# Optimization experiments

Hardware: AMD Instinct MI355X
Metric: run time of the kernel (lower is better)

Reference implementation:

```python
import jax, jax.numpy as jnp
import numpy as np


def setup_inputs() -> dict:
    key = jax.random.key(0)
    B, S, H, O, L, NH = 16, 1024, 1024, 256, 4, 8
    ks = jax.random.split(key, 10)
    s = 0.02
    return {
        "x": jax.random.normal(ks[0], (B, S, H), dtype=jnp.float32),
        "Wf": jax.random.normal(ks[1], (L, H, H), dtype=jnp.float32) * s,
        "bf": jnp.zeros((L, H), dtype=jnp.float32),
        "Wi": jax.random.normal(ks[2], (L, H, H), dtype=jnp.float32) * s,
        "bi": jnp.zeros((L, H), dtype=jnp.float32),
        "Wh": jax.random.normal(ks[3], (L, H, H), dtype=jnp.float32) * s,
        "bh": jnp.zeros((L, H), dtype=jnp.float32),
        "in_proj_w": jax.random.normal(ks[4], (3 * H, H), dtype=jnp.float32) * s,
        "in_proj_b": jnp.zeros((3 * H,), dtype=jnp.float32),
        "out_w": jax.random.normal(ks[5], (H, H), dtype=jnp.float32) * s,
        "out_b": jnp.zeros((H,), dtype=jnp.float32),
        "fc_w": jax.random.normal(ks[6], (O, H), dtype=jnp.float32) * s,
        "fc_b": jnp.zeros((O,), dtype=jnp.float32),
    }


def _min_lstm_layer(x, Wf, bf, Wi, bi, Wh, bh):
    # x: [B, S, D] -> [B, S, H]. minLSTM: h_t = f'_t * h_{t-1} + i'_t * h~_t
    f = jax.nn.sigmoid(jnp.einsum("bsd,hd->bsh", x, Wf) + bf)
    i = jax.nn.sigmoid(jnp.einsum("bsd,hd->bsh", x, Wi) + bi)
    h_tilde = jnp.einsum("bsd,hd->bsh", x, Wh) + bh
    denom = f + i
    fp = f / denom                      # decay coefficient per step
    add = (i / denom) * h_tilde         # input contribution per step
    # sequential scan over time (linear gated recurrence)
    def step(h, inp):
        fp_t, add_t = inp               # each [B, H]
        h = fp_t * h + add_t
        return h, h
    B, S, H = fp.shape
    h0 = jnp.zeros((B, H), dtype=x.dtype)
    _, hs = jax.lax.scan(step, h0, (fp.transpose(1, 0, 2), add.transpose(1, 0, 2)))
    return hs.transpose(1, 0, 2)        # [B, S, H]


def _mhsa(x, in_proj_w, in_proj_b, out_w, out_b, num_heads=8):
    B, S, H = x.shape
    dh = H // num_heads
    qkv = jnp.einsum("bsh,oh->bso", x, in_proj_w) + in_proj_b  # [B,S,3H]
    q, k, v = jnp.split(qkv, 3, axis=-1)
    def heads(t):
        return t.reshape(B, S, num_heads, dh).transpose(0, 2, 1, 3)  # [B,nh,S,dh]
    q, k, v = heads(q), heads(k), heads(v)
    scores = jnp.einsum("bnqd,bnkd->bnqk", q, k) / jnp.sqrt(jnp.float32(dh)).astype(x.dtype)
    attn = jax.nn.softmax(scores, axis=-1)
    o = jnp.einsum("bnqk,bnkd->bnqd", attn, v)
    o = o.transpose(0, 2, 1, 3).reshape(B, S, H)
    return jnp.einsum("bsh,oh->bso", o, out_w) + out_b


def reference(x, Wf, bf, Wi, bi, Wh, bh, in_proj_w, in_proj_b, out_w, out_b, fc_w, fc_b):
    out = x
    L = Wf.shape[0]
    for l in range(L):
        out = _min_lstm_layer(out, Wf[l], bf[l], Wi[l], bi[l], Wh[l], bh[l])
    attn_out = _mhsa(out, in_proj_w, in_proj_b, out_w, out_b, num_heads=8)
    out = attn_out + out                 # dropout is identity at eval
    last = out[:, -1, :]                 # [B, H]
    return jnp.einsum("bh,oh->bo", last, fc_w) + fc_b
```

## Files before the change

### kernel.cpp

```cpp
#include <hip/hip_runtime.h>
#include <hip/hip_bf16.h>
#include <math.h>

#define Bq   16
#define Sq   1024
#define Hq   1024
#define Oq   256
#define Lq   4
#define NHq  8
#define DHq  128
#define Mq   (Bq*Sq)
#define HHq  (Hq*Hq)
#define NCc  32
#define CTc  32

typedef __bf16 bf16x8 __attribute__((ext_vector_type(8)));
typedef float  f32x4  __attribute__((ext_vector_type(4)));

__device__ __forceinline__ float bf2f(unsigned int u) {
    union { unsigned int i; float f; } x; x.i = u << 16; return x.f;
}
__device__ __forceinline__ unsigned short f2bf(float f) {
    union { float f; unsigned int i; } x; x.f = f;
    unsigned int r = x.i + 0x7fffu + ((x.i >> 16) & 1u);
    return (unsigned short)(r >> 16);
}
__device__ __forceinline__ float sigm(float x) { return 1.f / (1.f + __expf(-x)); }

__device__ __forceinline__ void gl2lds16(const unsigned short* g, unsigned short* l) {
    __builtin_amdgcn_global_load_lds((const __attribute__((address_space(1))) void*)g,
                                     (__attribute__((address_space(3))) void*)l, 16, 0, 0);
}

__global__ void cvt_kernel(const float* __restrict__ src, unsigned short* __restrict__ dst, int n) {
    int i = blockIdx.x * 256 + threadIdx.x;
    if (i < n) dst[i] = f2bf(src[i]);
}

__global__ void cvtW_kernel(const float* __restrict__ Wf, const float* __restrict__ Wi,
                            const float* __restrict__ Wh, unsigned short* __restrict__ Wcat) {
    int i = blockIdx.x * 256 + threadIdx.x;
    int l = (i >> 20) / 3;
    int r = i - l * 3 * HHq;
    int g = r >> 20; int j = r & (HHq - 1);
    const float* s = (g == 0) ? Wf : (g == 1) ? Wi : Wh;
    Wcat[i] = f2bf(s[(size_t)l * HHq + j]);
}

__global__ void bias3_kernel(const float* __restrict__ bf_, const float* __restrict__ bi_,
                             const float* __restrict__ bh_, float* __restrict__ out) {
    int i = blockIdx.x * 256 + threadIdx.x;
    int l = i / (3*Hq); int r = i % (3*Hq); int g = r >> 10; int j = r & (Hq-1);
    const float* s = (g == 0) ? bf_ : (g == 1) ? bi_ : bh_;
    out[i] = s[l*Hq + j];
}

__global__ __launch_bounds__(256, 3)
void gemm_gate_kernel(const unsigned short* __restrict__ A, const unsigned short* __restrict__ Wl,
                      const float* __restrict__ bias3, unsigned short* __restrict__ FPo,
                      unsigned short* __restrict__ ADDo)
{
    const int K = Hq;
    __shared__ unsigned short As[2*4096];
    __shared__ unsigned short Ws[2*6144];
    const int tid  = threadIdx.x;

    const int lid = blockIdx.x;
    const int xcd = lid & 7;
    const int s   = lid >> 3;
    const int bm  = xcd * 16 + (s >> 4);
    const int cb  = s & 15;

    const int wid  = tid >> 6, lane = tid & 63;
    const int wm   = (wid >> 1) * 64;
    const int wn   = (wid & 1) * 32;
    const int l15  = lane & 15, quad = lane >> 4;

    const unsigned short* Ag = A + (size_t)(bm*128) * K;

    const int lr   = lane >> 2;
    const int gc   = (lane & 3) ^ ((lane >> 3) & 3);
    size_t offA[2]; int ldsA[2];
    #pragma unroll
    for (int q = 0; q < 2; ++q) {
        int ra = wid*32 + q*16 + lr;
        offA[q] = (size_t)ra * K + gc*8;
        ldsA[q] = (wid*32 + q*16) * 32;
    }
    size_t offW[3]; int ldsW[3];
    #pragma unroll
    for (int q = 0; q < 3; ++q) {
        int rw = wid*48 + q*16 + lr;
        int g  = rw >> 6;
        int nr = rw & 63;
        offW[q] = (size_t)g * HHq + (size_t)(cb*64 + nr) * K + gc*8;
        ldsW[q] = (wid*48 + q*16) * 32;
    }

    const int crd = quad ^ ((l15 >> 1) & 3);

    f32x4 acc[3][4][2] = {};

    const int niter = K >> 5;

    #pragma unroll
    for (int q = 0; q < 2; ++q) gl2lds16(Ag + offA[q], &As[ldsA[q]]);
    #pragma unroll
    for (int q = 0; q < 3; ++q) gl2lds16(Wl + offW[q], &Ws[ldsW[q]]);
    __syncthreads();

    for (int it = 0; it < niter; ++it) {
        const int cur = it & 1;
        if (it + 1 < niter) {
            const int nxt = (it + 1) & 1;
            const size_t k1 = (size_t)(it + 1) << 5;
            #pragma unroll
            for (int q = 0; q < 2; ++q) gl2lds16(Ag + offA[q] + k1, &As[nxt*4096 + ldsA[q]]);
            #pragma unroll
            for (int q = 0; q < 3; ++q) gl2lds16(Wl + offW[q] + k1, &Ws[nxt*6144 + ldsW[q]]);
        }
        bf16x8 af[4];
        #pragma unroll
        for (int t = 0; t < 4; ++t)
            af[t] = *(const bf16x8*)&As[cur*4096 + (wm + t*16 + l15)*32 + crd*8];
        #pragma unroll
        for (int g = 0; g < 3; ++g) {
            bf16x8 wf[2];
            #pragma unroll
            for (int t = 0; t < 2; ++t)
                wf[t] = *(const bf16x8*)&Ws[cur*6144 + (g*64 + wn + t*16 + l15)*32 + crd*8];
            #pragma unroll
            for (int tm = 0; tm < 4; ++tm)
                #pragma unroll
                for (int tn = 0; tn < 2; ++tn)
                    acc[g][tm][tn] = __builtin_amdgcn_mfma_f32_16x16x32_bf16(af[tm], wf[tn], acc[g][tm][tn], 0, 0, 0);
        }
        __syncthreads();
    }

    #pragma unroll
    for (int tm = 0; tm < 4; ++tm) {
        int row0 = bm*128 + wm + tm*16 + quad*4;
        #pragma unroll
        for (int tn = 0; tn < 2; ++tn) {
            int col = cb*64 + wn + tn*16 + l15;
            float bf_ = bias3[col], bi_ = bias3[Hq + col], bh_ = bias3[2*Hq + col];
            #pragma unroll
            for (int r = 0; r < 4; ++r) {
                float f  = sigm(acc[0][tm][tn][r] + bf_);
                float i  = sigm(acc[1][tm][tn][r] + bi_);
                float ht = acc[2][tm][tn][r] + bh_;
                float rd = 1.f / (f + i);
                size_t off = (size_t)(row0 + r) * Hq + col;
                FPo[off]  = f2bf(f * rd);
                ADDo[off] = f2bf(i * rd * ht);
            }
        }
    }
}

__global__ __launch_bounds__(256)
void gemm_bt_kernel(const unsigned short* __restrict__ A, const unsigned short* __restrict__ W,
                    const float* __restrict__ bias, unsigned short* __restrict__ C,
                    int N, int K, int nbn)
{
    __shared__ unsigned short As[2*4096];
    __shared__ unsigned short Ws[2*4096];
    const int tid  = threadIdx.x;

    const int lid = blockIdx.x;
    const int xcd = lid & 7;
    const int s   = lid >> 3;
    const int bm  = xcd * 16 + s / nbn;
    const int bn  = s % nbn;

    const int wid  = tid >> 6, lane = tid & 63;
    const int wm   = (wid >> 1) * 64, wn = (wid & 1) * 64;
    const int l15  = lane & 15, quad = lane >> 4;

    const unsigned short* Ag = A + (size_t)(bm*128) * K;
    const unsigned short* Wg = W + (size_t)(bn*128) * K;

    const int r0   = wid*32 + (lane >> 2);
    const int cst  = (lane & 3) ^ ((r0 >> 1) & 3);
    const size_t g0 = (size_t)r0 * K + cst*8;
    const size_t g1 = (size_t)(r0 + 16) * K + cst*8;
    const int lofs0 = wid*1024;
    const int lofs1 = wid*1024 + 512;

    const int crd = quad ^ ((l15 >> 1) & 3);

    f32x4 acc[4][4] = {};

    const int niter = K >> 5;

    gl2lds16(Ag + g0, &As[lofs0]);
    gl2lds16(Ag + g1, &As[lofs1]);
    gl2lds16(Wg + g0, &Ws[lofs0]);
    gl2lds16(Wg + g1, &Ws[lofs1]);
    __syncthreads();

    for (int it = 0; it < niter; ++it) {
        const int cur = it & 1;
        if (it + 1 < niter) {
            const int nxt = (it + 1) & 1;
            const size_t k1 = (size_t)(it + 1) << 5;
            gl2lds16(Ag + g0 + k1, &As[nxt*4096 + lofs0]);
            gl2lds16(Ag + g1 + k1, &As[nxt*4096 + lofs1]);
            gl2lds16(Wg + g0 + k1, &Ws[nxt*4096 + lofs0]);
            gl2lds16(Wg + g1 + k1, &Ws[nxt*4096 + lofs1]);
        }
        bf16x8 af[4], wf[4];
        #pragma unroll
        for (int t = 0; t < 4; ++t) {
            af[t] = *(const bf16x8*)&As[cur*4096 + (wm + t*16 + l15)*32 + crd*8];
            wf[t] = *(const bf16x8*)&Ws[cur*4096 + (wn + t*16 + l15)*32 + crd*8];
        }
        #pragma unroll
        for (int tm = 0; tm < 4; ++tm)
            #pragma unroll
            for (int tn = 0; tn < 4; ++tn)
                acc[tm][tn] = __builtin_amdgcn_mfma_f32_16x16x32_bf16(af[tm], wf[tn], acc[tm][tn], 0, 0, 0);
        __syncthreads();
    }

    #pragma unroll
    for (int tm = 0; tm < 4; ++tm) {
        int row0 = bm*128 + wm + tm*16 + quad*4;
        #pragma unroll
        for (int tn = 0; tn < 4; ++tn) {
            int col = bn*128 + wn + tn*16 + l15;
            float bv = bias[col];
            #pragma unroll
            for (int r = 0; r < 4; ++r)
                C[(size_t)(row0 + r) * N + col] = f2bf(acc[tm][tn][r] + bv);
        }
    }
}

__global__ __launch_bounds__(256)
void scan_sum_kernel(const unsigned short* __restrict__ FP, const unsigned short* __restrict__ AD,
                     float* __restrict__ Ps, float* __restrict__ Asum) {
    int bid = blockIdx.x;
    int tid = threadIdx.x;
    int b = bid >> 6; int r = bid & 63; int chunk = r >> 1; int jb = r & 1;
    int j = jb*512 + tid*2;
    size_t base = ((size_t)(b*Sq + chunk*CTc)) * Hq + j;
    float P0 = 1.f, P1 = 1.f, A0 = 0.f, A1 = 0.f;
    for (int s = 0; s < CTc; ++s) {
        size_t ro = base + (size_t)s * Hq;
        unsigned int uf = *(const unsigned int*)(FP + ro);
        unsigned int ua = *(const unsigned int*)(AD + ro);
        float fp0 = bf2f(uf & 0xffffu), fp1 = bf2f(uf >> 16);
        float ad0 = bf2f(ua & 0xffffu), ad1 = bf2f(ua >> 16);
        P0 *= fp0; A0 = fp0 * A0 + ad0;
        P1 *= fp1; A1 = fp1 * A1 + ad1;
    }
    int oi = (b*NCc + chunk)*Hq + j;
    Ps[oi] = P0; Ps[oi+1] = P1;
    Asum[oi] = A0; Asum[oi+1] = A1;
}

__global__ void scan_base_kernel(const float* __restrict__ Ps, const float* __restrict__ Asum,
                                 float* __restrict__ Hb) {
    int t = blockIdx.x * 256 + threadIdx.x;
    int b = t >> 10, j = t & 1023;
    float h = 0.f;
    for (int c = 0; c < NCc; ++c) {
        int idx = (b*NCc + c)*Hq + j;
        Hb[idx] = h;
        h = Ps[idx] * h + Asum[idx];
    }
}

__global__ __launch_bounds__(256)
void scan_out_kernel(const unsigned short* __restrict__ FP, const unsigned short* __restrict__ AD,
                     const float* __restrict__ Hb, unsigned short* __restrict__ Ho) {
    int bid = blockIdx.x;
    int tid = threadIdx.x;
    int b = bid >> 6; int r = bid & 63; int chunk = r >> 1; int jb = r & 1;
    int j = jb*512 + tid*2;
    size_t base = ((size_t)(b*Sq + chunk*CTc)) * Hq + j;
    int oi = (b*NCc + chunk)*Hq + j;
    float h0 = Hb[oi], h1 = Hb[oi+1];
    for (int s = 0; s < CTc; ++s) {
        size_t ro = base + (size_t)s * Hq;
        unsigned int uf = *(const unsigned int*)(FP + ro);
        unsigned int ua = *(const unsigned int*)(AD + ro);
        h0 = bf2f(uf & 0xffffu) * h0 + bf2f(ua & 0xffffu);
        h1 = bf2f(uf >> 16)     * h1 + bf2f(ua >> 16);
        unsigned int packed = (unsigned int)f2bf(h0) | ((unsigned int)f2bf(h1) << 16);
        *(unsigned int*)(Ho + ro) = packed;
    }
}

__global__ void xlast_kernel(const unsigned short* __restrict__ act, float* __restrict__ xl) {
    int i = blockIdx.x * 256 + threadIdx.x;
    int b = i >> 10, j = i & 1023;
    xl[i] = bf2f((unsigned int)act[((size_t)(b*Sq + Sq-1)) * Hq + j]);
}

__global__ __launch_bounds__(256)
void gemv_kernel(const float* __restrict__ W, const float* __restrict__ xv,
                 const float* __restrict__ bias, const float* __restrict__ resid,
                 float* __restrict__ out, int N) {
    int b = blockIdx.x;
    int w = threadIdx.x >> 6, lane = threadIdx.x & 63;
    int n = blockIdx.y*4 + w;
    __shared__ float xs[Hq];
    *(float4*)&xs[threadIdx.x*4] = *(const float4*)&xv[(size_t)b*Hq + threadIdx.x*4];
    __syncthreads();
    const float4* wr = (const float4*)(W + (size_t)n * Hq);
    float a = 0.f;
    #pragma unroll
    for (int c = 0; c < 4; ++c) {
        float4 wv = wr[c*64 + lane];
        float4 x4 = *(const float4*)&xs[c*256 + lane*4];
        a += wv.x*x4.x + wv.y*x4.y + wv.z*x4.z + wv.w*x4.w;
    }
    #pragma unroll
    for (int st = 32; st > 0; st >>= 1) a += __shfl_xor(a, st, 64);
    if (lane == 0) out[(size_t)b*N + n] = a + bias[n] + (resid ? resid[(size_t)b*Hq + n] : 0.f);
}

__global__ __launch_bounds__(1024)
void attn_kernel(const unsigned short* __restrict__ KV,
                 const float* __restrict__ q, float* __restrict__ o) {
    int b = blockIdx.x >> 3, nh = blockIdx.x & 7;
    int tid = threadIdx.x;
    __shared__ float qs[DHq];
    __shared__ float p[Sq];
    __shared__ float redw[16];
    __shared__ float red2[16*DHq];
    if (tid < DHq) qs[tid] = q[b*Hq + nh*DHq + tid] * 0.08838834764831845f;
    __syncthreads();

    const int g = tid >> 4, l = tid & 15;
    const unsigned short* Kb = KV + (size_t)b*Sq*2048 + nh*DHq;
    float lmax = -1e30f;
    #pragma unroll 4
    for (int it = 0; it < 16; ++it) {
        int s = it*64 + g;
        union { uint4 v; unsigned short u[8]; } kk;
        kk.v = *(const uint4*)(Kb + (size_t)s*2048 + l*8);
        float a = 0.f;
        #pragma unroll
        for (int j = 0; j < 8; ++j) a += bf2f((unsigned int)kk.u[j]) * qs[l*8 + j];
        a += __shfl_xor(a, 1, 16);
        a += __shfl_xor(a, 2, 16);
        a += __shfl_xor(a, 4, 16);
        a += __shfl_xor(a, 8, 16);
        if (l == 0) p[s] = a;
        lmax = fmaxf(lmax, a);
    }
    #pragma unroll
    for (int st = 32; st > 0; st >>= 1) lmax = fmaxf(lmax, __shfl_xor(lmax, st, 64));
    if ((tid & 63) == 0) redw[tid >> 6] = lmax;
    __syncthreads();
    float mx = redw[0];
    #pragma unroll
    for (int i = 1; i < 16; ++i) mx = fmaxf(mx, redw[i]);

    float e = __expf(p[tid] - mx);
    float ls = e;
    #pragma unroll
    for (int st = 32; st > 0; st >>= 1) ls += __shfl_xor(ls, st, 64);
    __syncthreads();
    p[tid] = e;
    if ((tid & 63) == 0) redw[tid >> 6] = ls;
    __syncthreads();
    float ssum = 0.f;
    #pragma unroll
    for (int i = 0; i < 16; ++i) ssum += redw[i];
    float inv = 1.f / ssum;

    int d2 = (tid & 63) * 2, sb = tid >> 6;
    const unsigned short* Vb = KV + (size_t)b*Sq*2048 + 1024 + nh*DHq + d2;
    float a0 = 0.f, a1 = 0.f;
    for (int s = sb*64; s < sb*64 + 64; ++s) {
        unsigned int vv = *(const unsigned int*)(Vb + (size_t)s*2048);
        float pw = p[s];
        a0 += pw * bf2f(vv & 0xffffu);
        a1 += pw * bf2f(vv >> 16);
    }
    red2[sb*DHq + d2] = a0;
    red2[sb*DHq + d2 + 1] = a1;
    __syncthreads();
    if (tid < DHq) {
        float a = 0.f;
        #pragma unroll
        for (int i = 0; i < 16; ++i) a += red2[i*DHq + tid];
        o[b*Hq + nh*DHq + tid] = a * inv;
    }
}

extern "C" void kernel_launch(void* const* d_in, const int* in_sizes, int n_in,
                              void* d_out, int out_size, void* d_ws, size_t ws_size,
                              hipStream_t stream) {
    const float* x        = (const float*)d_in[0];
    const float* Wf       = (const float*)d_in[1];
    const float* bfv      = (const float*)d_in[2];
    const float* Wi       = (const float*)d_in[3];
    const float* biv      = (const float*)d_in[4];
    const float* Wh       = (const float*)d_in[5];
    const float* bhv      = (const float*)d_in[6];
    const float* in_proj_w= (const float*)d_in[7];
    const float* in_proj_b= (const float*)d_in[8];
    const float* out_w    = (const float*)d_in[9];
    const float* out_b    = (const float*)d_in[10];
    const float* fc_w     = (const float*)d_in[11];
    const float* fc_b     = (const float*)d_in[12];
    float* outp = (float*)d_out;

    char* p = (char*)d_ws;
    auto alloc = [&](size_t bytes) -> void* {
        void* r = (void*)p; p += (bytes + 255) & ~(size_t)255; return r;
    };
    unsigned short* Wcat = (unsigned short*)alloc((size_t)Lq*3*HHq*2);
    unsigned short* Wkv  = (unsigned short*)alloc((size_t)2048*Hq*2);
    float*          Bias3= (float*)alloc((size_t)Lq*3*Hq*4);
    unsigned short* actA = (unsigned short*)alloc((size_t)Mq*Hq*2);
    unsigned short* actB = (unsigned short*)alloc((size_t)Mq*Hq*2);
    unsigned short* FPg  = (unsigned short*)alloc((size_t)Mq*Hq*2);
    unsigned short* ADDg = (unsigned short*)alloc((size_t)Mq*Hq*2);
    float* Ps   = (float*)alloc((size_t)Bq*NCc*Hq*4);
    float* Asum = (float*)alloc((size_t)Bq*NCc*Hq*4);
    float* Hb   = (float*)alloc((size_t)Bq*NCc*Hq*4);
    unsigned short* KV = FPg;
    float* xl   = (float*)alloc((size_t)Bq*Hq*4);
    float* qbuf = (float*)alloc((size_t)Bq*Hq*4);
    float* obuf = (float*)alloc((size_t)Bq*Hq*4);
    float* rbuf = (float*)alloc((size_t)Bq*Hq*4);

    cvt_kernel<<<Mq*Hq/256, 256, 0, stream>>>(x, actA, Mq*Hq);
    cvtW_kernel<<<Lq*3*HHq/256, 256, 0, stream>>>(Wf, Wi, Wh, Wcat);
    cvt_kernel<<<2048*Hq/256, 256, 0, stream>>>(in_proj_w + (size_t)Hq*Hq, Wkv, 2048*Hq);
    bias3_kernel<<<(Lq*3*Hq)/256, 256, 0, stream>>>(bfv, biv, bhv, Bias3);

    unsigned short* cur = actA;
    unsigned short* nxt = actB;
    for (int l = 0; l < Lq; ++l) {
        gemm_gate_kernel<<<(Mq/128)*16, 256, 0, stream>>>(
            cur, Wcat + (size_t)l*3*HHq, Bias3 + l*3*Hq, FPg, ADDg);
        scan_sum_kernel<<<Bq*NCc*2, 256, 0, stream>>>(FPg, ADDg, Ps, Asum);
        scan_base_kernel<<<Bq*Hq/256, 256, 0, stream>>>(Ps, Asum, Hb);
        scan_out_kernel<<<Bq*NCc*2, 256, 0, stream>>>(FPg, ADDg, Hb, nxt);
        unsigned short* t = cur; cur = nxt; nxt = t;
    }

    gemm_bt_kernel<<<(Mq/128)*(2048/128), 256, 0, stream>>>(
        cur, Wkv, in_proj_b + Hq, KV, 2048, Hq, 2048/128);
    xlast_kernel<<<Bq*Hq/256, 256, 0, stream>>>(cur, xl);
    gemv_kernel<<<dim3(Bq, Hq/4), 256, 0, stream>>>(in_proj_w, xl, in_proj_b, nullptr, qbuf, Hq);
    attn_kernel<<<Bq*NHq, 1024, 0, stream>>>(KV, qbuf, obuf);
    gemv_kernel<<<dim3(Bq, Hq/4), 256, 0, stream>>>(out_w, obuf, out_b, xl, rbuf, Hq);
    gemv_kernel<<<dim3(Bq, Oq/4), 256, 0, stream>>>(fc_w, rbuf, fc_b, nullptr, outp, Oq);
}
```

Measured before the change: 917.9 us.

## Enlarge gate GEMM tile to 128x384 with 512 threads and 4-stage LDS pipeline

The fused gate GEMM now uses 512-thread blocks covering 128 hidden columns per gate instead of 64, which halves the grid and increases reuse of A tiles. The double-buffered loop is replaced by a 4-slot LDS ring with two stages prefetched ahead, explicit vmcnt waits and raw barriers, and s_setprio raised around the MFMA block. This aims to hide global-load latency and cut per-tile overhead, at the cost of 128KB of LDS per block and lower occupancy.

```diff
diff --git a/kernel.cpp b/kernel.cpp
--- a/kernel.cpp
+++ b/kernel.cpp
@@ -55,95 +55,107 @@
     out[i] = s[l*Hq + j];
 }
 
-__global__ __launch_bounds__(256, 3)
+__global__ __launch_bounds__(512, 2)
 void gemm_gate_kernel(const unsigned short* __restrict__ A, const unsigned short* __restrict__ Wl,
                       const float* __restrict__ bias3, unsigned short* __restrict__ FPo,
                       unsigned short* __restrict__ ADDo)
 {
     const int K = Hq;
-    __shared__ unsigned short As[2*4096];
-    __shared__ unsigned short Ws[2*6144];
+    __shared__ unsigned short lds[4 * 16384];
     const int tid  = threadIdx.x;
 
     const int lid = blockIdx.x;
     const int xcd = lid & 7;
     const int s   = lid >> 3;
-    const int bm  = xcd * 16 + (s >> 4);
-    const int cb  = s & 15;
+    const int bm  = xcd * 16 + (s >> 3);
+    const int cb  = s & 7;
 
     const int wid  = tid >> 6, lane = tid & 63;
-    const int wm   = (wid >> 1) * 64;
-    const int wn   = (wid & 1) * 32;
+    const int wm   = (wid >> 2) * 64;
+    const int wn   = (wid & 3) * 32;
     const int l15  = lane & 15, quad = lane >> 4;
 
     const unsigned short* Ag = A + (size_t)(bm*128) * K;
 
-    const int lr   = lane >> 2;
-    const int gc   = (lane & 3) ^ ((lane >> 3) & 3);
-    size_t offA[2]; int ldsA[2];
-    #pragma unroll
-    for (int q = 0; q < 2; ++q) {
-        int ra = wid*32 + q*16 + lr;
-        offA[q] = (size_t)ra * K + gc*8;
-        ldsA[q] = (wid*32 + q*16) * 32;
-    }
-    size_t offW[3]; int ldsW[3];
+    const int lr = lane >> 2;
+    const int gc = (lane & 3) ^ ((lane >> 3) & 3);
+
+    const int offA = (wid*16 + lr) * K + gc*8;
+    const int ldsA = wid * 512;
+    int offW[3], ldsW[3];
     #pragma unroll
     for (int q = 0; q < 3; ++q) {
         int rw = wid*48 + q*16 + lr;
-        int g  = rw >> 6;
-        int nr = rw & 63;
-        offW[q] = (size_t)g * HHq + (size_t)(cb*64 + nr) * K + gc*8;
-        ldsW[q] = (wid*48 + q*16) * 32;
+        int g  = rw >> 7;
+        int nr = rw & 127;
+        offW[q] = g * HHq + (cb*128 + nr) * K + gc*8;
+        ldsW[q] = 4096 + (wid*48 + q*16) * 32;
     }
 
     const int crd = quad ^ ((l15 >> 1) & 3);
 
     f32x4 acc[3][4][2] = {};
 
-    const int niter = K >> 5;
-
-    #pragma unroll
-    for (int q = 0; q < 2; ++q) gl2lds16(Ag + offA[q], &As[ldsA[q]]);
-    #pragma unroll
-    for (int q = 0; q < 3; ++q) gl2lds16(Wl + offW[q], &Ws[ldsW[q]]);
-    __syncthreads();
-
-    for (int it = 0; it < niter; ++it) {
-        const int cur = it & 1;
-        if (it + 1 < niter) {
-            const int nxt = (it + 1) & 1;
-            const size_t k1 = (size_t)(it + 1) << 5;
-            #pragma unroll
-            for (int q = 0; q < 2; ++q) gl2lds16(Ag + offA[q] + k1, &As[nxt*4096 + ldsA[q]]);
-            #pragma unroll
-            for (int q = 0; q < 3; ++q) gl2lds16(Wl + offW[q] + k1, &Ws[nxt*6144 + ldsW[q]]);
-        }
+    auto STAGE = [&](int kt, int slot) {
+        const int kof = kt << 5;
+        unsigned short* Sb = &lds[slot * 16384];
+        gl2lds16(Ag + offA + kof,    Sb + ldsA);
+        gl2lds16(Wl + offW[0] + kof, Sb + ldsW[0]);
+        gl2lds16(Wl + offW[1] + kof, Sb + ldsW[1]);
+        gl2lds16(Wl + offW[2] + kof, Sb + ldsW[2]);
+    };
+
+    auto COMPUTE = [&](int slot) {
+        const unsigned short* Sa = &lds[slot * 16384];
+        const unsigned short* Sw = Sa + 4096;
         bf16x8 af[4];
         #pragma unroll
         for (int t = 0; t < 4; ++t)
-            af[t] = *(const bf16x8*)&As[cur*4096 + (wm + t*16 + l15)*32 + crd*8];
-        #pragma unroll
-        for (int g = 0; g < 3; ++g) {
-            bf16x8 wf[2];
+            af[t] = *(const bf16x8*)&Sa[(wm + t*16 + l15)*32 + crd*8];
+        bf16x8 wf[3][2];
+        #pragma unroll
+        for (int g = 0; g < 3; ++g)
             #pragma unroll
             for (int t = 0; t < 2; ++t)
-                wf[t] = *(const bf16x8*)&Ws[cur*6144 + (g*64 + wn + t*16 + l15)*32 + crd*8];
+                wf[g][t] = *(const bf16x8*)&Sw[(g*128 + wn + t*16 + l15)*32 + crd*8];
+        __builtin_amdgcn_s_setprio(1);
+        #pragma unroll
+        for (int g = 0; g < 3; ++g)
             #pragma unroll
             for (int tm = 0; tm < 4; ++tm)
                 #pragma unroll
                 for (int tn = 0; tn < 2; ++tn)
-                    acc[g][tm][tn] = __builtin_amdgcn_mfma_f32_16x16x32_bf16(af[tm], wf[tn], acc[g][tm][tn], 0, 0, 0);
-        }
-        __syncthreads();
-    }
+                    acc[g][tm][tn] = __builtin_amdgcn_mfma_f32_16x16x32_bf16(af[tm], wf[g][tn], acc[g][tm][tn], 0, 0, 0);
+        __builtin_amdgcn_s_setprio(0);
+    };
+
+    const int niter = K >> 5;
+
+    STAGE(0, 0);
+    STAGE(1, 1);
+
+    for (int t = 0; t < niter - 2; ++t) {
+        STAGE(t + 2, (t + 2) & 3);
+        asm volatile("s_waitcnt vmcnt(8) lgkmcnt(0)" ::: "memory");
+        __builtin_amdgcn_s_barrier();
+        asm volatile("" ::: "memory");
+        COMPUTE(t & 3);
+    }
+    asm volatile("s_waitcnt vmcnt(4) lgkmcnt(0)" ::: "memory");
+    __builtin_amdgcn_s_barrier();
+    asm volatile("" ::: "memory");
+    COMPUTE((niter - 2) & 3);
+    asm volatile("s_waitcnt vmcnt(0) lgkmcnt(0)" ::: "memory");
+    __builtin_amdgcn_s_barrier();
+    asm volatile("" ::: "memory");
+    COMPUTE((niter - 1) & 3);
 
     #pragma unroll
     for (int tm = 0; tm < 4; ++tm) {
         int row0 = bm*128 + wm + tm*16 + quad*4;
         #pragma unroll
         for (int tn = 0; tn < 2; ++tn) {
-            int col = cb*64 + wn + tn*16 + l15;
+            int col = cb*128 + wn + tn*16 + l15;
             float bf_ = bias3[col], bi_ = bias3[Hq + col], bh_ = bias3[2*Hq + col];
             #pragma unroll
             for (int r = 0; r < 4; ++r) {
@@ -440,7 +452,7 @@
     unsigned short* cur = actA;
     unsigned short* nxt = actB;
     for (int l = 0; l < Lq; ++l) {
-        gemm_gate_kernel<<<(Mq/128)*16, 256, 0, stream>>>(
+        gemm_gate_kernel<<<(Mq/128)*(Hq/128), 512, 0, stream>>>(
             cur, Wcat + (size_t)l*3*HHq, Bias3 + l*3*Hq, FPg, ADDg);
         scan_sum_kernel<<<Bq*NCc*2, 256, 0, stream>>>(FPg, ADDg, Ps, Asum);
         scan_base_kernel<<<Bq*Hq/256, 256, 0, stream>>>(Ps, Asum, Hb);
```

New measurement: 876.5 us. 4.5% less time.
